# Kernel optimization log

Measured on AMD Instinct MI355X. Metric: run time of the kernel, lower is better.

The kernel has to match this reference:

```python
import jax, jax.numpy as jnp
import numpy as np

BN_EPS = 1e-5
LEAKY_SLOPE = 0.1


def conv_bn_leaky(x, w, gamma, beta, mean, var, pad):
    # Conv2d(no bias) + BatchNorm2d(inference) + LeakyReLU(0.1), NCHW/OIHW
    y = jax.lax.conv_general_dilated(
        x, w, window_strides=(1, 1), padding=[(pad, pad), (pad, pad)],
        dimension_numbers=("NCHW", "OIHW", "NCHW"))
    scale = gamma / jnp.sqrt(var + BN_EPS)
    shift = beta - mean * scale
    y = y * scale[None, :, None, None] + shift[None, :, None, None]
    return jnp.where(y > 0, y, LEAKY_SLOPE * y)


def reorg(x, s=2):
    # vedanet Reorg: out[b, (a*s+d)*C + c, i, j] = x[b, c, i*s+a, j*s+d]
    B, C, H, W = x.shape
    Ho, Wo = H // s, W // s
    return x.reshape(B, C, Ho, s, Wo, s).transpose(0, 3, 5, 1, 2, 4).reshape(B, s * s * C, Ho, Wo)


def setup_inputs() -> dict:
    key = jax.random.key(0)
    ks = jax.random.split(key, 10)
    B, H, W = 32, 19, 19
    NC, NA = 20, 5
    return {
        "stage6": jax.random.normal(ks[0], (B, 1024, H, W), jnp.float32),
        "stage5": jax.random.normal(ks[1], (B, 512, 2 * H, 2 * W), jnp.float32),
        "w1": jax.random.normal(ks[2], (64, 512, 1, 1), jnp.float32) * 0.05,
        "g1": jnp.ones((64,), jnp.float32),
        "b1": jnp.zeros((64,), jnp.float32),
        "m1": jax.random.normal(ks[3], (64,), jnp.float32) * 0.1,
        "v1": jax.random.uniform(ks[4], (64,), jnp.float32, 0.5, 1.5),
        "w2": jax.random.normal(ks[5], (1024, 1280, 3, 3), jnp.float32) * 0.02,
        "g2": jnp.ones((1024,), jnp.float32),
        "b2": jnp.zeros((1024,), jnp.float32),
        "m2": jax.random.normal(ks[6], (1024,), jnp.float32) * 0.1,
        "v2": jax.random.uniform(ks[7], (1024,), jnp.float32, 0.5, 1.5),
        "meta_state": jax.random.normal(ks[8], (NC, NA * 6, 1025), jnp.float32) * 0.05,
    }


def reference(stage6, stage5, w1, g1, b1, m1, v1, w2, g2, b2, m2, v2, meta_state):
    # layers[0]: 1x1 conv-bn-leaky on stage5, then Reorg(2) -> (B, 256, H, W)
    x = conv_bn_leaky(stage5, w1, g1, b1, m1, v1, pad=0)
    x = reorg(x, 2)
    # layers[1]: 3x3 conv-bn-leaky on concat -> (B, 1024, H, W)
    pre = conv_bn_leaky(jnp.concatenate([x, stage6], axis=1), w2, g2, b2, m2, v2, pad=1)
    # meta_predict: per-class 1x1 conv, batched as one einsum
    cls_w = meta_state[:, :, :-1]   # (NC, NA*6, 1024)
    cls_b = meta_state[:, :, -1]    # (NC, NA*6)
    out = jnp.einsum("bkij,cmk->bcmij", pre, cls_w) + cls_b[None, :, :, None, None]
    B, NC, M = pre.shape[0], meta_state.shape[0], meta_state.shape[1]
    return out.reshape(B * NC, M, pre.shape[2], pre.shape[3])
```

## Files before the change

### kernel.cpp

```cpp
#include <hip/hip_runtime.h>

typedef unsigned short u16;
typedef unsigned int   u32;

typedef __attribute__((ext_vector_type(8))) short bf16x8;
typedef __attribute__((ext_vector_type(4))) float f32x4;

__device__ __forceinline__ u16 f2bf(float f) {
  u32 u = __float_as_uint(f);
  u32 r = (u + 0x7fffu + ((u >> 16) & 1u)) >> 16;
  return (u16)r;
}

__device__ __forceinline__ void async16(const void* g, void* l) {
  __builtin_amdgcn_global_load_lds(
      (const __attribute__((address_space(1))) u32*)g,
      (__attribute__((address_space(3))) u32*)l, 16, 0, 0);
}

__global__ __launch_bounds__(256) void mega_prep_kern(
    const float* __restrict__ stage5, const float* __restrict__ s6,
    const float* __restrict__ w1,
    const float* __restrict__ g1, const float* __restrict__ b1,
    const float* __restrict__ m1, const float* __restrict__ v1,
    const float* __restrict__ w2, const float* __restrict__ g2,
    const float* __restrict__ b2, const float* __restrict__ m2,
    const float* __restrict__ v2, const float* __restrict__ meta,
    u16* __restrict__ in_bf, u16* __restrict__ w2p,
    u16* __restrict__ clsp, float* __restrict__ clsb,
    float* __restrict__ shift2)
{
  __shared__ __align__(16) char smem[18816];
  const int bid = blockIdx.x;
  const int t = threadIdx.x;

  if (bid < 722) {
    float* sc_s = (float*)smem;
    float* sh_s = (float*)(smem + 256);
    char*  aT   = smem + 512;
    char*  bT   = smem + 4608;
    const int w = t >> 6, lane = t & 63;
    if (t < 64) {
      float s = g1[t] * rsqrtf(v1[t] + 1e-5f);
      sc_s[t] = s;
      sh_s[t] = b1[t] - m1[t] * s;
    }
    const int m0 = bid * 64;
    const int pS = t & 63, gS = t >> 6;
    const int mS = m0 + pS;
    const int bS = mS / 1444, hwS = mS - bS * 1444;
    const float* s5 = stage5 + (size_t)bS * (512 * 1444) + hwS;
    const int ocA = t >> 2, icqA = t & 3;
    const float* w1r = w1 + (size_t)ocA * 512 + icqA * 8;
    char* aW = aT + (ocA >> 4) * 1024 + (icqA * 16 + (ocA & 15)) * 16;
    char* bW = bT + pS * 64 + ((gS ^ ((pS >> 1) & 3))) * 16;
    const int bR = (w * 16 + (lane & 15)) * 64 +
                   (((lane >> 4) ^ (((lane & 15) >> 1) & 3))) * 16;
    f32x4 acc[4] = {};
    __syncthreads();
    const float sA = sc_s[ocA];
    for (int kc = 0; kc < 16; ++kc) {
      const int ic0 = kc * 32;
      float a8[8], b8[8];
#pragma unroll
      for (int e = 0; e < 8; ++e) a8[e] = w1r[ic0 + e];
#pragma unroll
      for (int e = 0; e < 8; ++e) b8[e] = s5[(size_t)(ic0 + gS * 8 + e) * 1444];
      __syncthreads();
      uint4 av, bv;
      av.x = (u32)f2bf(a8[0] * sA) | ((u32)f2bf(a8[1] * sA) << 16);
      av.y = (u32)f2bf(a8[2] * sA) | ((u32)f2bf(a8[3] * sA) << 16);
      av.z = (u32)f2bf(a8[4] * sA) | ((u32)f2bf(a8[5] * sA) << 16);
      av.w = (u32)f2bf(a8[6] * sA) | ((u32)f2bf(a8[7] * sA) << 16);
      bv.x = (u32)f2bf(b8[0]) | ((u32)f2bf(b8[1]) << 16);
      bv.y = (u32)f2bf(b8[2]) | ((u32)f2bf(b8[3]) << 16);
      bv.z = (u32)f2bf(b8[4]) | ((u32)f2bf(b8[5]) << 16);
      bv.w = (u32)f2bf(b8[6]) | ((u32)f2bf(b8[7]) << 16);
      *(uint4*)aW = av;
      *(uint4*)bW = bv;
      __syncthreads();
      bf16x8 bfv = *(const bf16x8*)(bT + bR);
#pragma unroll
      for (int i = 0; i < 4; ++i) {
        bf16x8 af = *(const bf16x8*)(aT + i * 1024 + lane * 16);
        acc[i] = __builtin_amdgcn_mfma_f32_16x16x32_bf16(af, bfv, acc[i], 0, 0, 0);
      }
    }
    const int mE = m0 + w * 16 + (lane & 15);
    const int bE = mE / 1444, hwE = mE - bE * 1444;
    const int h = hwE / 38, wq = hwE - h * 38;
    const int ho = h >> 1, wo = wq >> 1, q = ((h & 1) << 1) | (wq & 1);
    u16* dst = in_bf + (((size_t)bE * 21 + 1 + ho) * 21 + 1 + wo) * 1280 + q * 64;
    const int lq = lane >> 4;
#pragma unroll
    for (int i = 0; i < 4; ++i) {
      int oc = i * 16 + lq * 4;
      float v0 = acc[i][0] + sh_s[oc + 0]; v0 = v0 > 0.f ? v0 : 0.1f * v0;
      float v1_ = acc[i][1] + sh_s[oc + 1]; v1_ = v1_ > 0.f ? v1_ : 0.1f * v1_;
      float v2_ = acc[i][2] + sh_s[oc + 2]; v2_ = v2_ > 0.f ? v2_ : 0.1f * v2_;
      float v3 = acc[i][3] + sh_s[oc + 3]; v3 = v3 > 0.f ? v3 : 0.1f * v3;
      u32 lo = (u32)f2bf(v0) | ((u32)f2bf(v1_) << 16);
      u32 hi = (u32)f2bf(v2_) | ((u32)f2bf(v3) << 16);
      u32* dp = (u32*)(dst + oc);
      dp[0] = lo; dp[1] = hi;
    }
    return;
  }

  if (bid < 3794) {
    u16 (*tile)[66] = (u16(*)[66])smem;
    const int sub = bid - 722;
    const int jt = sub % 6, ct = (sub / 6) % 16, b = sub / 96;
    const int ij0 = jt * 64, c0 = ct * 64;
    const int col = t & 63, rr = t >> 6;
#pragma unroll
    for (int r = 0; r < 16; ++r) {
      int cl = r * 4 + rr;
      int ij = ij0 + col;
      float v = 0.f;
      if (ij < 361) v = s6[((size_t)b * 1024 + c0 + cl) * 361 + ij];
      tile[cl][col] = f2bf(v);
    }
    __syncthreads();
#pragma unroll
    for (int r = 0; r < 16; ++r) {
      int ijl = r * 4 + rr;
      int ij = ij0 + ijl;
      if (ij < 361) {
        int i = ij / 19, j = ij - i * 19;
        in_bf[(((size_t)b * 21 + 1 + i) * 21 + 1 + j) * 1280 + 256 + c0 + col] =
            tile[col][ijl];
      }
    }
    return;
  }

  if (bid < 5394) {
    int gi = (bid - 3794) * 256 + t;
    int b = gi / 12800;
    int rem = gi - b * 12800;
    int p = rem / 160, qq = rem - p * 160;
    int row, col;
    if (p < 21)      { row = 0;      col = p; }
    else if (p < 42) { row = 20;     col = p - 21; }
    else if (p < 61) { row = p - 41; col = 0; }
    else             { row = p - 60; col = 20; }
    uint4 z = {0u, 0u, 0u, 0u};
    *(uint4*)(in_bf + (((size_t)b * 21 + row) * 21 + col) * 1280 + qq * 8) = z;
    return;
  }

  if (bid < 5694) {
    int idx = (bid - 5394) * 256 + t;
    int cm = idx >> 7, a = idx & 127;
    int kc = a >> 2, ksub = a & 3;
    int tile_ = cm >> 7, g = (cm >> 4) & 7, mm = cm & 15;
    const float* srcp = meta + (size_t)cm * 1025 + a * 8;
    uint4 v;
    v.x = (u32)f2bf(srcp[0]) | ((u32)f2bf(srcp[1]) << 16);
    v.y = (u32)f2bf(srcp[2]) | ((u32)f2bf(srcp[3]) << 16);
    v.z = (u32)f2bf(srcp[4]) | ((u32)f2bf(srcp[5]) << 16);
    v.w = (u32)f2bf(srcp[6]) | ((u32)f2bf(srcp[7]) << 16);
    size_t dst = (((size_t)tile_ * 32 + kc) * 8 + g) * 512
                 + (size_t)(ksub * 16 + mm) * 8;
    *(uint4*)(clsp + dst) = v;
    if (idx < 600) clsb[idx] = meta[(size_t)idx * 1025 + 1024];
    if (idx < 1024) {
      float sc = g2[idx] * rsqrtf(v2[idx] + 1e-5f);
      shift2[idx] = b2[idx] - m2[idx] * sc;
    }
    return;
  }

  {
    u16* tile = (u16*)smem;
    float* sc_s = (float*)(smem + 18720);
    const int sub = bid - 5694;
    const int icb = sub % 10;
    const int oc0 = (sub / 10) * 8;
    if (t < 8) sc_s[t] = g2[oc0 + t] * rsqrtf(v2[oc0 + t] + 1e-5f);
    __syncthreads();
    const float* src = w2 + (size_t)oc0 * 11520 + (size_t)icb * 128 * 9;
#pragma unroll
    for (int r = 0; r < 36; ++r) {
      int p = r * 256 + t;
      int oc_l = p / 1152, rem = p - oc_l * 1152;
      int ic_l = rem / 9, khw = rem - ic_l * 9;
      tile[oc_l * 1170 + khw * 130 + ic_l] =
          f2bf(src[(size_t)oc_l * 11520 + rem] * sc_s[oc_l]);
    }
    __syncthreads();
#pragma unroll
    for (int r = 0; r < 5; ++r) {
      int wi = r * 256 + t;
      if (wi < 1152) {
        int oc_l = wi / 144, q = wi - oc_l * 144;
        int khw = q >> 4, c = (q >> 2) & 3, ksub = q & 3;
        int oc = oc0 + oc_l;
        int kt = khw * 40 + icb * 4 + c;
        const u16* s = &tile[oc_l * 1170 + khw * 130 + c * 32 + ksub * 8];
        uint4 v;
        v.x = (u32)s[0] | ((u32)s[1] << 16);
        v.y = (u32)s[2] | ((u32)s[3] << 16);
        v.z = (u32)s[4] | ((u32)s[5] << 16);
        v.w = (u32)s[6] | ((u32)s[7] << 16);
        size_t dst = (((size_t)(oc >> 8) * 360 + kt) * 2 + ((oc & 255) >> 7)) * 4096
                     + (size_t)(((oc >> 4) & 7) * 64 + ksub * 16 + (oc & 15)) * 8;
        *(uint4*)(w2p + dst) = v;
      }
    }
  }
}

__global__ __launch_bounds__(512, 2) void conv2_gemm_kern(
    const u16* __restrict__ Wp, const u16* __restrict__ Ig,
    const float* __restrict__ shift2, u16* __restrict__ pre)
{
  __shared__ u16 As[4][8192];
  __shared__ u16 Bs[4][6144];
  __shared__ float shft[256];

  const int t = threadIdx.x;
  const int w = t >> 6, lane = t & 63;
  const int wm = w >> 2, wn = w & 3;

  const int xcd = blockIdx.x & 7, sub8 = blockIdx.x >> 3;
  const int s = (xcd < 4 ? xcd * 31 : 124 + (xcd - 4) * 30) + sub8;
  const int mTile = s >> 2, ocTile = s & 3;
  const int m0 = mTile * 192, oc0 = ocTile * 256;

  const int rw = t >> 2;
  const int rpart = ((t & 3) ^ ((t >> 3) & 3)) * 8;
  int mA = m0 + rw;        if (mA > 11551) mA = 11551;
  int mB = m0 + 128 + rw;  if (mB > 11551) mB = 11551;
  const int bA = mA / 361, ijA = mA - bA * 361;
  const int ohA = ijA / 19, owA = ijA - ohA * 19;
  const int bB = mB / 361, ijB = mB - bB * 361;
  const int ohB = ijB / 19, owB = ijB - ohB * 19;
  const u16* pI0 = Ig + (size_t)((bA * 21 + ohA) * 21 + owA) * 1280 + rpart;
  const u16* pI1 = Ig + (size_t)((bB * 21 + ohB) * 21 + owB) * 1280 + rpart;

  const u16* pW = Wp + (size_t)ocTile * 2949120 + (size_t)t * 8;

  const int aOff = wm * 4096 + lane * 8;
  const int bOff = (wn * 48 + (lane & 15)) * 32 +
                   (((lane >> 4) ^ ((lane >> 1) & 3)) * 8);

  int skh = 0, skw = 0, sicb = 0, sIo = 0;

#pragma unroll
  for (int st = 0; st < 3; ++st) {
    async16(pW + (size_t)st * 8192,        &As[st][t * 8]);
    async16(pI0 + sIo,                     &Bs[st][t * 8]);
    async16(pW + (size_t)st * 8192 + 4096, &As[st][4096 + t * 8]);
    if (w < 4) async16(pI1 + sIo,          &Bs[st][4096 + t * 8]);
    ++sicb; sIo += 32;
    if (sicb == 40) { sicb = 0; ++skw; if (skw == 3) { skw = 0; ++skh; }
                      sIo = (skh * 21 + skw) * 1280; }
  }
  asm volatile("s_waitcnt vmcnt(6)" ::: "memory");
  __builtin_amdgcn_s_barrier();

  f32x4 acc[8][3] = {};

  for (int kq = 0; kq < 90; ++kq) {
#pragma unroll
    for (int r = 0; r < 4; ++r) {
      const int kt = kq * 4 + r;
      const int cb = r;
      const int stb = (r + 3) & 3;
      const int st = (kt > 356) ? 359 : kt + 3;
      const size_t aSrc = (size_t)st * 8192;

      bf16x8 af0[4], af1[4], bfv[3];
#pragma unroll
      for (int i = 0; i < 4; ++i)
        af0[i] = *(const bf16x8*)&As[cb][aOff + i * 512];
#pragma unroll
      for (int j = 0; j < 3; ++j)
        bfv[j] = *(const bf16x8*)&Bs[cb][bOff + j * 512];
      async16(pW + aSrc, &As[stb][t * 8]);
      async16(pI0 + sIo, &Bs[stb][t * 8]);
#pragma unroll
      for (int i = 0; i < 4; ++i)
        af1[i] = *(const bf16x8*)&As[cb][aOff + 2048 + i * 512];
      async16(pW + aSrc + 4096, &As[stb][4096 + t * 8]);
      if (w < 4) async16(pI1 + sIo, &Bs[stb][4096 + t * 8]);

      asm volatile("s_waitcnt lgkmcnt(4)" ::: "memory");
      __builtin_amdgcn_sched_barrier(0);
      __builtin_amdgcn_s_setprio(1);
#pragma unroll
      for (int i = 0; i < 4; ++i)
#pragma unroll
        for (int j = 0; j < 3; ++j)
          acc[i][j] = __builtin_amdgcn_mfma_f32_16x16x32_bf16(
              af0[i], bfv[j], acc[i][j], 0, 0, 0);
      __builtin_amdgcn_s_setprio(0);

      asm volatile("s_waitcnt lgkmcnt(0)" ::: "memory");
      __builtin_amdgcn_sched_barrier(0);
      __builtin_amdgcn_s_setprio(1);
#pragma unroll
      for (int i = 0; i < 4; ++i)
#pragma unroll
        for (int j = 0; j < 3; ++j)
          acc[4 + i][j] = __builtin_amdgcn_mfma_f32_16x16x32_bf16(
              af1[i], bfv[j], acc[4 + i][j], 0, 0, 0);
      __builtin_amdgcn_s_setprio(0);

      asm volatile("s_waitcnt vmcnt(6)" ::: "memory");
      __builtin_amdgcn_s_barrier();

      ++sicb; sIo += 32;
      if (sicb == 40) { sicb = 0; ++skw; if (skw == 3) { skw = 0; ++skh; }
                        sIo = (skh * 21 + skw) * 1280; }
    }
  }

  if (t < 256) shft[t] = shift2[oc0 + t];
  __syncthreads();

  const int lq = lane >> 4, lr = lane & 15;
#pragma unroll
  for (int j = 0; j < 3; ++j) {
    const int m = m0 + wn * 48 + j * 16 + lr;
    if (m >= 11552) continue;
    u16* prow = pre + (size_t)m * 1024 + oc0 + wm * 128;
#pragma unroll
    for (int i = 0; i < 8; ++i) {
      const int ocl = i * 16 + lq * 4;
      float v0 = acc[i][j][0] + shft[wm * 128 + ocl + 0]; v0 = v0 > 0.f ? v0 : 0.1f * v0;
      float v1 = acc[i][j][1] + shft[wm * 128 + ocl + 1]; v1 = v1 > 0.f ? v1 : 0.1f * v1;
      float v2 = acc[i][j][2] + shft[wm * 128 + ocl + 2]; v2 = v2 > 0.f ? v2 : 0.1f * v2;
      float v3 = acc[i][j][3] + shft[wm * 128 + ocl + 3]; v3 = v3 > 0.f ? v3 : 0.1f * v3;
      u32 lo = (u32)f2bf(v0) | ((u32)f2bf(v1) << 16);
      u32 hi = (u32)f2bf(v2) | ((u32)f2bf(v3) << 16);
      u32* dp = (u32*)(prow + ocl);
      dp[0] = lo; dp[1] = hi;
    }
  }
}

__global__ __launch_bounds__(512) void einsum_gemm_kern(
    const u16* __restrict__ Ap, const u16* __restrict__ Bg,
    const float* __restrict__ biasg, float* __restrict__ out)
{
  __shared__ u16 Wa[3][4096];
  __shared__ u16 Ib[3][8192];
  __shared__ float sbias[128];
  const int t = threadIdx.x;
  const int w = t >> 6, lane = t & 63;
  const int q = w >> 1, ch = w & 1;
  const int m0 = blockIdx.x * 256;
  const int cm0 = blockIdx.y * 128;
  if (t < 128) { int c = cm0 + t; sbias[t] = (c < 600) ? biasg[c] : 0.f; }

  const u16* pA = Ap + (size_t)(cm0 >> 7) * (32 * 4096) + (size_t)t * 8;

  const int rw = t >> 2;
  const int rpart = ((t & 3) ^ ((t >> 3) & 3)) * 8;
  int rB0 = m0 + rw;        if (rB0 > 11551) rB0 = 11551;
  int rB1 = m0 + 128 + rw;  if (rB1 > 11551) rB1 = 11551;
  const u16* pB0 = Bg + (size_t)rB0 * 1024 + rpart;
  const u16* pB1 = Bg + (size_t)rB1 * 1024 + rpart;

  const int aBase = ch * 2048 + lane * 8;
  const int bBase = (q * 64 + (lane & 15)) * 32 +
                    (((lane >> 4) ^ ((lane >> 1) & 3))) * 8;

#pragma unroll
  for (int st = 0; st < 2; ++st) {
    const size_t off = (size_t)st * 32;
    async16(pA + (size_t)st * 4096, &Wa[st][t * 8]);
    async16(pB0 + off, &Ib[st][t * 8]);
    async16(pB1 + off, &Ib[st][4096 + t * 8]);
  }
  asm volatile("s_waitcnt vmcnt(3)" ::: "memory");
  __builtin_amdgcn_s_barrier();

  f32x4 acc[4][4] = {};

  for (int kt = 0; kt < 32; ++kt) {
    const int cb = kt % 3;
    const int stb = (kt + 2) % 3;
    const int st = (kt < 30) ? kt + 2 : 31;
    const size_t off = (size_t)st * 32;
    async16(pA + (size_t)st * 4096, &Wa[stb][t * 8]);
    async16(pB0 + off, &Ib[stb][t * 8]);
    async16(pB1 + off, &Ib[stb][4096 + t * 8]);

    bf16x8 af[4], bfv[4];
#pragma unroll
    for (int i = 0; i < 4; ++i)
      af[i] = *(const bf16x8*)&Wa[cb][aBase + i * 512];
#pragma unroll
    for (int j = 0; j < 4; ++j)
      bfv[j] = *(const bf16x8*)&Ib[cb][bBase + j * 512];
    asm volatile("s_waitcnt lgkmcnt(0)" ::: "memory");
    __builtin_amdgcn_sched_barrier(0);
    __builtin_amdgcn_s_setprio(1);
#pragma unroll
    for (int i = 0; i < 4; ++i)
#pragma unroll
      for (int j = 0; j < 4; ++j)
        acc[i][j] = __builtin_amdgcn_mfma_f32_16x16x32_bf16(
            af[i], bfv[j], acc[i][j], 0, 0, 0);
    __builtin_amdgcn_s_setprio(0);
    asm volatile("s_waitcnt vmcnt(3)" ::: "memory");
    __builtin_amdgcn_s_barrier();
  }

  const int lq = lane >> 4, lr = lane & 15;
#pragma unroll
  for (int j = 0; j < 4; ++j) {
    int m = m0 + q * 64 + j * 16 + lr;
    if (m >= 11552) continue;
    int b = m / 361, ij = m - b * 361;
    float* obase = out + (size_t)b * 216600 + ij;
#pragma unroll
    for (int i = 0; i < 4; ++i) {
      int cml = ch * 64 + i * 16 + lq * 4;
#pragma unroll
      for (int r = 0; r < 4; ++r) {
        int cm = cm0 + cml + r;
        if (cm < 600) obase[(size_t)cm * 361] = acc[i][j][r] + sbias[cml + r];
      }
    }
  }
}

extern "C" void kernel_launch(void* const* d_in, const int* in_sizes, int n_in,
                              void* d_out, int out_size, void* d_ws, size_t ws_size,
                              hipStream_t stream)
{
  const float* stage6 = (const float*)d_in[0];
  const float* stage5 = (const float*)d_in[1];
  const float* w1 = (const float*)d_in[2];
  const float* g1 = (const float*)d_in[3];
  const float* b1 = (const float*)d_in[4];
  const float* m1 = (const float*)d_in[5];
  const float* v1 = (const float*)d_in[6];
  const float* w2 = (const float*)d_in[7];
  const float* g2 = (const float*)d_in[8];
  const float* b2 = (const float*)d_in[9];
  const float* m2 = (const float*)d_in[10];
  const float* v2 = (const float*)d_in[11];
  const float* meta = (const float*)d_in[12];
  float* out = (float*)d_out;

  char* ws = (char*)d_ws;
  u16*   in_bf  = (u16*)(ws);
  u16*   w2p    = (u16*)(ws + 36126720);
  u16*   prebf  = (u16*)(ws + 59719680);
  u16*   clsp   = (u16*)(ws + 83378176);
  float* clsb   = (float*)(ws + 84688896);
  float* shift2 = (float*)(ws + 84691456);

  mega_prep_kern<<<6974, 256, 0, stream>>>(
      stage5, stage6, w1, g1, b1, m1, v1, w2, g2, b2, m2, v2, meta,
      in_bf, w2p, clsp, clsb, shift2);
  conv2_gemm_kern<<<244, 512, 0, stream>>>(w2p, in_bf, shift2, prebf);
  einsum_gemm_kern<<<dim3(46, 5), 512, 0, stream>>>(clsp, prebf, clsb, out);
}
```

Before: 520.0 us.

## Switch conv2 GEMM from 4-stage K32 ring to double-buffered K64 stages

Restructures the conv2 implicit-GEMM main loop from a four-deep ring of K=32 LDS stages to two buffers of K=64, halving the number of block barriers per K. Each iteration issues the next tile's loads in two halves interleaved with the MFMA sub-steps and then waits with vmcnt(0). This cuts barrier and loop overhead but reduces prefetch depth to one stage, so global-load latency may be exposed more.

```diff
diff --git a/kernel.cpp b/kernel.cpp
--- a/kernel.cpp
+++ b/kernel.cpp
@@ -216,8 +216,8 @@
     const u16* __restrict__ Wp, const u16* __restrict__ Ig,
     const float* __restrict__ shift2, u16* __restrict__ pre)
 {
-  __shared__ u16 As[4][8192];
-  __shared__ u16 Bs[4][6144];
+  __shared__ u16 As[2][16384];
+  __shared__ u16 Bs[2][12288];
   __shared__ float shft[256];
 
   const int t = threadIdx.x;
@@ -246,46 +246,44 @@
   const int bOff = (wn * 48 + (lane & 15)) * 32 +
                    (((lane >> 4) ^ ((lane >> 1) & 3)) * 8);
 
-  int skh = 0, skw = 0, sicb = 0, sIo = 0;
-
-#pragma unroll
-  for (int st = 0; st < 3; ++st) {
-    async16(pW + (size_t)st * 8192,        &As[st][t * 8]);
-    async16(pI0 + sIo,                     &Bs[st][t * 8]);
-    async16(pW + (size_t)st * 8192 + 4096, &As[st][4096 + t * 8]);
-    if (w < 4) async16(pI1 + sIo,          &Bs[st][4096 + t * 8]);
-    ++sicb; sIo += 32;
-    if (sicb == 40) { sicb = 0; ++skw; if (skw == 3) { skw = 0; ++skh; }
-                      sIo = (skh * 21 + skw) * 1280; }
-  }
-  asm volatile("s_waitcnt vmcnt(6)" ::: "memory");
+  async16(pW,                 &As[0][t * 8]);
+  async16(pW + 4096,          &As[0][4096 + t * 8]);
+  async16(pW + 8192,          &As[0][8192 + t * 8]);
+  async16(pW + 12288,         &As[0][12288 + t * 8]);
+  async16(pI0,                &Bs[0][t * 8]);
+  if (w < 4) async16(pI1,     &Bs[0][4096 + t * 8]);
+  async16(pI0 + 32,           &Bs[0][6144 + t * 8]);
+  if (w < 4) async16(pI1 + 32,&Bs[0][10240 + t * 8]);
+  asm volatile("s_waitcnt vmcnt(0)" ::: "memory");
   __builtin_amdgcn_s_barrier();
 
+  int skh = 0, skw = 0, sp = 1, sIo = 64;
+
   f32x4 acc[8][3] = {};
 
   for (int kq = 0; kq < 90; ++kq) {
 #pragma unroll
-    for (int r = 0; r < 4; ++r) {
-      const int kt = kq * 4 + r;
-      const int cb = r;
-      const int stb = (r + 3) & 3;
-      const int st = (kt > 356) ? 359 : kt + 3;
-      const size_t aSrc = (size_t)st * 8192;
-
-      bf16x8 af0[4], af1[4], bfv[3];
-#pragma unroll
-      for (int i = 0; i < 4; ++i)
-        af0[i] = *(const bf16x8*)&As[cb][aOff + i * 512];
+    for (int r = 0; r < 2; ++r) {
+      const int kt = kq * 2 + r;
+      const int cur = r, nxt = r ^ 1;
+      const int st = (kt < 179) ? kt + 1 : 179;
+      const size_t aSrc = (size_t)st * 16384;
+
+      bf16x8 a0[4], a1[4], bf[3];
+
+#pragma unroll
+      for (int i = 0; i < 4; ++i)
+        a0[i] = *(const bf16x8*)&As[cur][aOff + i * 512];
 #pragma unroll
       for (int j = 0; j < 3; ++j)
-        bfv[j] = *(const bf16x8*)&Bs[cb][bOff + j * 512];
-      async16(pW + aSrc, &As[stb][t * 8]);
-      async16(pI0 + sIo, &Bs[stb][t * 8]);
-#pragma unroll
-      for (int i = 0; i < 4; ++i)
-        af1[i] = *(const bf16x8*)&As[cb][aOff + 2048 + i * 512];
-      async16(pW + aSrc + 4096, &As[stb][4096 + t * 8]);
-      if (w < 4) async16(pI1 + sIo, &Bs[stb][4096 + t * 8]);
+        bf[j] = *(const bf16x8*)&Bs[cur][bOff + j * 512];
+      async16(pW + aSrc,        &As[nxt][t * 8]);
+      async16(pW + aSrc + 4096, &As[nxt][4096 + t * 8]);
+      async16(pI0 + sIo,        &Bs[nxt][t * 8]);
+      if (w < 4) async16(pI1 + sIo, &Bs[nxt][4096 + t * 8]);
+#pragma unroll
+      for (int i = 0; i < 4; ++i)
+        a1[i] = *(const bf16x8*)&As[cur][aOff + 2048 + i * 512];
 
       asm volatile("s_waitcnt lgkmcnt(4)" ::: "memory");
       __builtin_amdgcn_sched_barrier(0);
@@ -295,7 +293,7 @@
 #pragma unroll
         for (int j = 0; j < 3; ++j)
           acc[i][j] = __builtin_amdgcn_mfma_f32_16x16x32_bf16(
-              af0[i], bfv[j], acc[i][j], 0, 0, 0);
+              a0[i], bf[j], acc[i][j], 0, 0, 0);
       __builtin_amdgcn_s_setprio(0);
 
       asm volatile("s_waitcnt lgkmcnt(0)" ::: "memory");
@@ -306,15 +304,51 @@
 #pragma unroll
         for (int j = 0; j < 3; ++j)
           acc[4 + i][j] = __builtin_amdgcn_mfma_f32_16x16x32_bf16(
-              af1[i], bfv[j], acc[4 + i][j], 0, 0, 0);
+              a1[i], bf[j], acc[4 + i][j], 0, 0, 0);
       __builtin_amdgcn_s_setprio(0);
 
-      asm volatile("s_waitcnt vmcnt(6)" ::: "memory");
+#pragma unroll
+      for (int i = 0; i < 4; ++i)
+        a0[i] = *(const bf16x8*)&As[cur][8192 + aOff + i * 512];
+#pragma unroll
+      for (int j = 0; j < 3; ++j)
+        bf[j] = *(const bf16x8*)&Bs[cur][6144 + bOff + j * 512];
+      async16(pW + aSrc + 8192,  &As[nxt][8192 + t * 8]);
+      async16(pW + aSrc + 12288, &As[nxt][12288 + t * 8]);
+      async16(pI0 + sIo + 32,    &Bs[nxt][6144 + t * 8]);
+      if (w < 4) async16(pI1 + sIo + 32, &Bs[nxt][10240 + t * 8]);
+#pragma unroll
+      for (int i = 0; i < 4; ++i)
+        a1[i] = *(const bf16x8*)&As[cur][8192 + 2048 + aOff + i * 512];
+
+      asm volatile("s_waitcnt lgkmcnt(4)" ::: "memory");
+      __builtin_amdgcn_sched_barrier(0);
+      __builtin_amdgcn_s_setprio(1);
+#pragma unroll
+      for (int i = 0; i < 4; ++i)
+#pragma unroll
+        for (int j = 0; j < 3; ++j)
+          acc[i][j] = __builtin_amdgcn_mfma_f32_16x16x32_bf16(
+              a0[i], bf[j], acc[i][j], 0, 0, 0);
+      __builtin_amdgcn_s_setprio(0);
+
+      asm volatile("s_waitcnt lgkmcnt(0)" ::: "memory");
+      __builtin_amdgcn_sched_barrier(0);
+      __builtin_amdgcn_s_setprio(1);
+#pragma unroll
+      for (int i = 0; i < 4; ++i)
+#pragma unroll
+        for (int j = 0; j < 3; ++j)
+          acc[4 + i][j] = __builtin_amdgcn_mfma_f32_16x16x32_bf16(
+              a1[i], bf[j], acc[4 + i][j], 0, 0, 0);
+      __builtin_amdgcn_s_setprio(0);
+
+      asm volatile("s_waitcnt vmcnt(0)" ::: "memory");
       __builtin_amdgcn_s_barrier();
 
-      ++sicb; sIo += 32;
-      if (sicb == 40) { sicb = 0; ++skw; if (skw == 3) { skw = 0; ++skh; }
-                        sIo = (skh * 21 + skw) * 1280; }
+      ++sp; sIo += 64;
+      if (sp == 20) { sp = 0; ++skw; if (skw == 3) { skw = 0; ++skh; }
+                      sIo = (skh * 21 + skw) * 1280; }
     }
   }
 
```

New measurement: 520.5 us, median of 3. About the same (+0.1%).
